# Kernel tuning notes

Hardware: AMD Instinct MI355X
Metric: run time of the kernel (lower is better)

The kernel has to match this reference:

```python
import jax, jax.numpy as jnp
import numpy as np

N0, N1, N2 = 100000, 20000, 4000   # src(block0), dst(block0)=src(block1), dst(block1)
R = 3                               # number of relations
E0, E1 = 160000, 64000              # edges per relation per block
IN_FEATS, HID = 128, 128
TSS, RS = 64, 64
NTOT = 200000                       # global node count for tss/rs embed tables
F_IN = HID + TSS + RS               # IGConv input feature dim = 256


def _lin(key, fi, fo):
    k1, k2 = jax.random.split(key)
    s = float(1.0 / np.sqrt(fi))
    w = jax.random.uniform(k1, (fi, fo), minval=-s, maxval=s, dtype=jnp.float32)
    b = jax.random.uniform(k2, (fo,), minval=-s, maxval=s, dtype=jnp.float32)
    return w, b


def setup_inputs() -> dict:
    ks = jax.random.split(jax.random.key(0), 32)
    inp = {}
    inp["x_user"] = jax.random.normal(ks[0], (N0, IN_FEATS), dtype=jnp.float32)
    inp["tss_embed"] = jax.random.normal(ks[1], (NTOT, TSS), dtype=jnp.float32)
    inp["rs_embed"] = jax.random.normal(ks[2], (NTOT, RS), dtype=jnp.float32)
    inp["src_nid0"] = jax.random.randint(ks[3], (N0,), 0, NTOT)
    inp["src_nid1"] = jax.random.randint(ks[4], (N1,), 0, NTOT)
    inp["e0_src"] = jax.random.randint(ks[5], (R, E0), 0, N0)
    inp["e0_dst"] = jax.random.randint(ks[6], (R, E0), 0, N1)
    inp["e1_src"] = jax.random.randint(ks[7], (R, E1), 0, N1)
    inp["e1_dst"] = jax.random.randint(ks[8], (R, E1), 0, N2)
    inp["embed_w"], inp["embed_b"] = _lin(ks[9], IN_FEATS, HID)
    i = 10
    for l in (1, 2):
        for nm, fi in (("fc1", F_IN), ("fc2", 3 * F_IN), ("fc3", 2 * HID)):
            pw, pb = zip(*[_lin(jax.random.fold_in(ks[i], r), fi, HID) for r in range(R)])
            inp["l%d_%s_w" % (l, nm)] = jnp.stack(pw)  # [R, fi, HID]
            inp["l%d_%s_b" % (l, nm)] = jnp.stack(pb)  # [R, HID]
            i += 1
    inp["attn_w1"], inp["attn_b1"] = _lin(ks[i], HID, HID)
    inp["attn_w2"] = _lin(ks[i + 1], HID, 1)[0]  # Linear(hid,1,bias=False)
    inp["pred_w"], inp["pred_b"] = _lin(ks[i + 2], HID, 1)
    return inp


def _igconv(src_feat, dst_feat, esrc, edst, n_dst, fc1w, fc1b, fc2w, fc2b, fc3w, fc3b):
    # copy_u gather then max/mean/sum segment reductions over destination nodes
    m = src_feat[esrc]                                   # [E, F]
    s = jax.ops.segment_sum(m, edst, num_segments=n_dst)
    deg = jax.ops.segment_sum(jnp.ones(esrc.shape, m.dtype), edst, num_segments=n_dst)
    mean = s / jnp.maximum(deg, 1.0)[:, None]
    mx = jax.ops.segment_max(m, edst, num_segments=n_dst)
    mx = jnp.where(deg[:, None] > 0, mx, jnp.zeros_like(mx))  # DGL zeros for isolated dst
    msg = jnp.concatenate([mx, mean, s], axis=1)         # [n_dst, 3F]
    inp = jnp.concatenate([msg @ fc2w + fc2b, dst_feat @ fc1w + fc1b], axis=1)
    return jax.nn.relu(inp) @ fc3w + fc3b                # [n_dst, HID]


def _attn(z, w1, b1, w2):
    # SemanticAttention: z [N, R, HID]
    w = (jnp.tanh(z @ w1 + b1) @ w2).mean(0)             # [R, 1]
    beta = jax.nn.softmax(w, axis=0)                     # [R, 1]
    return (beta[None] * z).sum(1)                       # [N, HID]


def _forward(x_user, tss_embed, rs_embed, embed_w, embed_b,
             l1_fc1_w, l1_fc1_b, l1_fc2_w, l1_fc2_b, l1_fc3_w, l1_fc3_b,
             l2_fc1_w, l2_fc1_b, l2_fc2_w, l2_fc2_b, l2_fc3_w, l2_fc3_b,
             attn_w1, attn_b1, attn_w2, pred_w, pred_b,
             src_nid0, src_nid1, e0_src, e0_dst, e1_src, e1_dst):
    u0 = x_user @ embed_w + embed_b                      # self.embed
    feat0 = jnp.concatenate([u0, tss_embed[src_nid0], rs_embed[src_nid0]], axis=1)  # [N0,256]
    conv1 = jax.vmap(lambda es, ed, w1, b1, w2, b2, w3, b3:
                     _igconv(feat0, feat0[:N1], es, ed, N1, w1, b1, w2, b2, w3, b3))
    z1 = conv1(e0_src, e0_dst, l1_fc1_w, l1_fc1_b, l1_fc2_w, l1_fc2_b, l1_fc3_w, l1_fc3_b)  # [R,N1,HID]
    h1 = jax.nn.relu(_attn(jnp.transpose(z1, (1, 0, 2)), attn_w1, attn_b1, attn_w2))  # [N1,HID]
    feat1 = jnp.concatenate([h1, tss_embed[src_nid1], rs_embed[src_nid1]], axis=1)    # [N1,256]
    conv2 = jax.vmap(lambda es, ed, w1, b1, w2, b2, w3, b3:
                     _igconv(feat1, feat1[:N2], es, ed, N2, w1, b1, w2, b2, w3, b3))
    z2 = conv2(e1_src, e1_dst, l2_fc1_w, l2_fc1_b, l2_fc2_w, l2_fc2_b, l2_fc3_w, l2_fc3_b)  # [R,N2,HID]
    h2 = _attn(jnp.transpose(z2, (1, 0, 2)), attn_w1, attn_b1, attn_w2)              # [N2,HID]
    return jax.nn.sigmoid(h2 @ pred_w + pred_b)          # [N2,1]


def reference(x_user, tss_embed, rs_embed, src_nid0, src_nid1,
              e0_src, e0_dst, e1_src, e1_dst, embed_w, embed_b,
              l1_fc1_w, l1_fc1_b, l1_fc2_w, l1_fc2_b, l1_fc3_w, l1_fc3_b,
              l2_fc1_w, l2_fc1_b, l2_fc2_w, l2_fc2_b, l2_fc3_w, l2_fc3_b,
              attn_w1, attn_b1, attn_w2, pred_w, pred_b):
    return _forward(x_user, tss_embed, rs_embed, embed_w, embed_b,
                    l1_fc1_w, l1_fc1_b, l1_fc2_w, l1_fc2_b, l1_fc3_w, l1_fc3_b,
                    l2_fc1_w, l2_fc1_b, l2_fc2_w, l2_fc2_b, l2_fc3_w, l2_fc3_b,
                    attn_w1, attn_b1, attn_w2, pred_w, pred_b,
                    src_nid0, src_nid1, e0_src, e0_dst, e1_src, e1_dst)
```

## Files before the change

kernel.cpp:

```cpp
#include <hip/hip_runtime.h>
#include <math.h>


typedef short s16x8 __attribute__((ext_vector_type(8)));
typedef float f32x4 __attribute__((ext_vector_type(4)));

__device__ __forceinline__ ushort f2bf(float f) {
  unsigned u = __float_as_uint(f);
  return (ushort)((u + 0x7FFFu + ((u >> 16) & 1u)) >> 16);
}
__device__ __forceinline__ float bf2f(unsigned hbits) {
  return __uint_as_float(hbits << 16);
}
__device__ __forceinline__ unsigned pack2(float lo, float hi) {
  return (unsigned)f2bf(lo) | ((unsigned)f2bf(hi) << 16);
}

struct PrepAll {
  const float* src[8];
  ushort* dst[8];
  int K[8];
  int total[8];
};

__global__ __launch_bounds__(256) void prep_all(PrepAll P)
{
  int t = blockIdx.z;
  int off = blockIdx.x * 256 + threadIdx.x;
  if (off >= P.total[t]) return;
  int K = P.K[t];
  int k = off % K;
  int n = (off / K) & 127;
  int r = off / (K * 128);
  P.dst[t][off] = f2bf(P.src[t][((size_t)r * K + k) * 128 + n]);
}

struct GemmDesc {
  const void* A; int lda; size_t aStride; int aKind;
  const ushort* Wt; size_t wStride;
  const float* bias; int biasStride;
  void* C; int ldc; size_t cStride; int cKind;
  int M, K, relu;
  const ushort* aggM; const ushort* aggS; const float* invdeg;
  size_t aggStride; int invStride;
  const int* gnid; const float* gtss; const float* grs;
};

template<int AKIND>
__device__ __forceinline__ uint4 loadA(const void* Ab, const ushort* AgM,
                                       const ushort* AgS, int lda, int row,
                                       bool rowOK, int k0, int quad, float idg)
{
  uint4 pk = make_uint4(0u, 0u, 0u, 0u);
  if (rowOK) {
    if constexpr (AKIND == 1) {
      pk = *(const uint4*)((const ushort*)Ab + (size_t)row * lda + k0 + quad * 8);
    } else if constexpr (AKIND == 0) {
      const float* A32 = (const float*)Ab;
      float4 fa = *(const float4*)(A32 + (size_t)row * lda + k0 + quad * 8);
      float4 fb = *(const float4*)(A32 + (size_t)row * lda + k0 + quad * 8 + 4);
      pk.x = pack2(fa.x, fa.y); pk.y = pack2(fa.z, fa.w);
      pk.z = pack2(fb.x, fb.y); pk.w = pack2(fb.z, fb.w);
    } else {
      int seg = k0 >> 8;
      int jj  = (k0 & 255) + quad * 8;
      const ushort* Ag = (seg == 0) ? AgM : AgS;
      pk = *(const uint4*)(Ag + (size_t)row * 256 + jj);
      if (seg == 1) {
        pk.x = pack2(bf2f(pk.x & 0xFFFFu) * idg, bf2f(pk.x >> 16) * idg);
        pk.y = pack2(bf2f(pk.y & 0xFFFFu) * idg, bf2f(pk.y >> 16) * idg);
        pk.z = pack2(bf2f(pk.z & 0xFFFFu) * idg, bf2f(pk.z >> 16) * idg);
        pk.w = pack2(bf2f(pk.w & 0xFFFFu) * idg, bf2f(pk.w >> 16) * idg);
      }
    }
  }
  return pk;
}

template<int K, int AKIND>
__device__ __forceinline__ void gemm_core(const GemmDesc& d, int r, ushort* Bs)
{
  constexpr int NC = K / 64;
  constexpr int NF = K / 32;

  const int tid = threadIdx.x;
  const int wave = tid >> 6, lane = tid & 63;
  const int m16 = lane & 15, quad = lane >> 4;
  const int rowBase = blockIdx.x * 64;
  const int row = rowBase + wave * 16 + m16;
  const bool rowOK = row < d.M;
  const ushort* Wt = d.Wt + (size_t)r * d.wStride;

  const void* Ab = (const char*)d.A +
      (size_t)r * d.aStride * (AKIND == 0 ? sizeof(float) : sizeof(ushort));
  const ushort* AgM = d.aggM + (size_t)r * d.aggStride;
  const ushort* AgS = d.aggS + (size_t)r * d.aggStride;

  float idg = 1.f;
  if (AKIND == 2 && rowOK) idg = d.invdeg[(size_t)r * d.invStride + row];

  f32x4 acc[8];
  #pragma unroll
  for (int j = 0; j < 8; ++j)
    #pragma unroll
    for (int p = 0; p < 4; ++p) acc[j][p] = 0.f;

  uint4 pkAll[(K <= 256) ? NF : 2];
  if constexpr (K <= 256) {
    #pragma unroll
    for (int f = 0; f < NF; ++f)
      pkAll[f] = loadA<AKIND>(Ab, AgM, AgS, d.lda, row, rowOK, f * 32, quad, idg);
  }

  #pragma unroll
  for (int c = 0; c < NC; ++c) {
    if constexpr (K > 256) {
      pkAll[0] = loadA<AKIND>(Ab, AgM, AgS, d.lda, row, rowOK, c * 64,      quad, idg);
      pkAll[1] = loadA<AKIND>(Ab, AgM, AgS, d.lda, row, rowOK, c * 64 + 32, quad, idg);
    }
    if (c) __syncthreads();
    #pragma unroll
    for (int i = 0; i < 4; ++i) {
      int q = tid + 256 * i;
      int col = ((q >> 6) & 7) * 16 + (q & 15);
      int kk  = c * 64 + ((q >> 9) & 1) * 32 + ((q >> 4) & 3) * 8;
      *(uint4*)&Bs[q * 8] = *(const uint4*)(Wt + (size_t)col * K + kk);
    }
    __syncthreads();

    #pragma unroll
    for (int ks = 0; ks < 2; ++ks) {
      uint4 pk = (K <= 256) ? pkAll[c * 2 + ks] : pkAll[ks];
      s16x8 af = *(s16x8*)&pk;
      #pragma unroll
      for (int j = 0; j < 8; ++j) {
        s16x8 bf = *(const s16x8*)&Bs[((ks * 8 + j) * 64 + lane) * 8];
        acc[j] = __builtin_amdgcn_mfma_f32_16x16x32_bf16(af, bf, acc[j], 0, 0, 0);
      }
    }
  }

  const float* bias = d.bias + (size_t)r * d.biasStride;
  float bcol[8];
  #pragma unroll
  for (int j = 0; j < 8; ++j) bcol[j] = bias[j * 16 + m16];

  #pragma unroll
  for (int p = 0; p < 4; ++p) {
    int grow = rowBase + wave * 16 + quad * 4 + p;
    if (grow >= d.M) continue;
    if (d.cKind == 0) {
      float* Crow = (float*)d.C + (size_t)r * d.cStride + (size_t)grow * d.ldc;
      #pragma unroll
      for (int j = 0; j < 8; ++j) {
        float v = acc[j][p] + bcol[j];
        if (d.relu) v = fmaxf(v, 0.f);
        Crow[j * 16 + m16] = v;
      }
    } else {
      ushort* Crow = (ushort*)d.C + (size_t)r * d.cStride + (size_t)grow * d.ldc;
      #pragma unroll
      for (int j = 0; j < 8; ++j) {
        float v = acc[j][p] + bcol[j];
        if (d.relu) v = fmaxf(v, 0.f);
        Crow[j * 16 + m16] = f2bf(v);
      }
    }
  }

  if constexpr (K == 128) {
    if (d.gnid) {
      #pragma unroll
      for (int i = 0; i < 8; ++i) {
        int q = tid + 256 * i;
        int grow = rowBase + (q >> 5);
        int c = q & 31;
        if (grow >= d.M) continue;
        int id = d.gnid[grow];
        float4 v = (c < 16) ? *(const float4*)(d.gtss + (size_t)id * 64 + c * 4)
                            : *(const float4*)(d.grs  + (size_t)id * 64 + (c - 16) * 4);
        uint2 g; g.x = pack2(v.x, v.y); g.y = pack2(v.z, v.w);
        *(uint2*)((ushort*)d.C + (size_t)grow * d.ldc + 128 + c * 4) = g;
      }
    }
  }
}

__global__ __launch_bounds__(256, 4) void gemm_mfma(GemmDesc d0, GemmDesc d1)
{
  __shared__ __align__(16) ushort Bs[1024 * 8];
  const GemmDesc& d = blockIdx.z ? d1 : d0;
  const int r = blockIdx.y;
  if (d.K == 128)      gemm_core<128, 0>(d, r, Bs);
  else if (d.K == 256) gemm_core<256, 1>(d, r, Bs);
  else                 gemm_core<768, 2>(d, r, Bs);
}

__global__ __launch_bounds__(256) void fc3_attn(
    const ushort* __restrict__ inp, size_t aStride,
    const ushort* __restrict__ wt3, size_t wStride,
    const float* __restrict__ b3,
    float* __restrict__ z, size_t zStride, int M,
    const ushort* __restrict__ w1t, const float* __restrict__ b1,
    const float* __restrict__ w2, float* __restrict__ wsum)
{
  __shared__ __align__(16) ushort Zs[64 * 128];
  __shared__ __align__(16) ushort Ws[1024 * 8];

  const int tid = threadIdx.x;
  const int wave = tid >> 6, lane = tid & 63;
  const int m16 = lane & 15, quad = lane >> 4;
  const int r = blockIdx.y;
  const int rowBase = blockIdx.x * 64;
  const int row = rowBase + wave * 16 + m16;
  const bool rowOK = row < M;

  const ushort* A  = inp + (size_t)r * aStride;
  const ushort* Wt = wt3 + (size_t)r * wStride;

  f32x4 acc[8];
  #pragma unroll
  for (int j = 0; j < 8; ++j)
    #pragma unroll
    for (int p = 0; p < 4; ++p) acc[j][p] = 0.f;

  uint4 pkAll[8];
  #pragma unroll
  for (int f = 0; f < 8; ++f) {
    uint4 pk = make_uint4(0u, 0u, 0u, 0u);
    if (rowOK) pk = *(const uint4*)(A + (size_t)row * 256 + f * 32 + quad * 8);
    pkAll[f] = pk;
  }

  #pragma unroll
  for (int c = 0; c < 4; ++c) {
    if (c) __syncthreads();
    #pragma unroll
    for (int i = 0; i < 4; ++i) {
      int q = tid + 256 * i;
      int col = ((q >> 6) & 7) * 16 + (q & 15);
      int kk  = c * 64 + ((q >> 9) & 1) * 32 + ((q >> 4) & 3) * 8;
      *(uint4*)&Ws[q * 8] = *(const uint4*)(Wt + (size_t)col * 256 + kk);
    }
    __syncthreads();
    #pragma unroll
    for (int ks = 0; ks < 2; ++ks) {
      s16x8 af = *(s16x8*)&pkAll[c * 2 + ks];
      #pragma unroll
      for (int j = 0; j < 8; ++j) {
        s16x8 bf = *(const s16x8*)&Ws[((ks * 8 + j) * 64 + lane) * 8];
        acc[j] = __builtin_amdgcn_mfma_f32_16x16x32_bf16(af, bf, acc[j], 0, 0, 0);
      }
    }
  }

  const float* bias = b3 + (size_t)r * 128;
  float bcol[8];
  #pragma unroll
  for (int j = 0; j < 8; ++j) bcol[j] = bias[j * 16 + m16];

  #pragma unroll
  for (int p = 0; p < 4; ++p) {
    int lrow = wave * 16 + quad * 4 + p;
    int grow = rowBase + lrow;
    bool ok = grow < M;
    float* Zr = z + (size_t)r * zStride + (size_t)grow * 128;
    #pragma unroll
    for (int j = 0; j < 8; ++j) {
      float v = ok ? acc[j][p] + bcol[j] : 0.f;
      if (ok) Zr[j * 16 + m16] = v;
      int byte = lrow * 256 + (j * 16 + m16) * 2;
      byte ^= (lrow & 7) << 4;
      *(ushort*)((char*)Zs + byte) = f2bf(v);
    }
  }

  f32x4 acc2[8];
  #pragma unroll
  for (int j = 0; j < 8; ++j)
    #pragma unroll
    for (int p = 0; p < 4; ++p) acc2[j][p] = 0.f;

  const int arow = wave * 16 + m16;
  #pragma unroll
  for (int c = 0; c < 2; ++c) {
    __syncthreads();
    #pragma unroll
    for (int i = 0; i < 4; ++i) {
      int q = tid + 256 * i;
      int col = ((q >> 6) & 7) * 16 + (q & 15);
      int kk  = c * 64 + ((q >> 9) & 1) * 32 + ((q >> 4) & 3) * 8;
      *(uint4*)&Ws[q * 8] = *(const uint4*)(w1t + (size_t)col * 128 + kk);
    }
    __syncthreads();
    #pragma unroll
    for (int ks = 0; ks < 2; ++ks) {
      int kk = c * 64 + ks * 32 + quad * 8;
      int byte = arow * 256 + kk * 2;
      byte ^= (arow & 7) << 4;
      s16x8 af = *(const s16x8*)((const char*)Zs + byte);
      #pragma unroll
      for (int j = 0; j < 8; ++j) {
        s16x8 bf = *(const s16x8*)&Ws[((ks * 8 + j) * 64 + lane) * 8];
        acc2[j] = __builtin_amdgcn_mfma_f32_16x16x32_bf16(af, bf, acc2[j], 0, 0, 0);
      }
    }
  }

  float b1c[8], w2c[8];
  #pragma unroll
  for (int j = 0; j < 8; ++j) { b1c[j] = b1[j * 16 + m16]; w2c[j] = w2[j * 16 + m16]; }

  float local = 0.f;
  #pragma unroll
  for (int p = 0; p < 4; ++p) {
    int grow = rowBase + wave * 16 + quad * 4 + p;
    if (grow >= M) continue;
    #pragma unroll
    for (int j = 0; j < 8; ++j)
      local += tanhf(acc2[j][p] + b1c[j]) * w2c[j];
  }
  #pragma unroll
  for (int o = 32; o > 0; o >>= 1) local += __shfl_down(local, o);
  __shared__ float red[4];
  if (lane == 0) red[wave] = local;
  __syncthreads();
  if (tid == 0) atomicAdd(&wsum[r], red[0] + red[1] + red[2] + red[3]);
}

__global__ void count_deg(const int* __restrict__ edst, int E, int N, int* __restrict__ deg)
{
  int e = blockIdx.x * blockDim.x + threadIdx.x;
  int r = blockIdx.y;
  if (e < E) atomicAdd(&deg[r * N + edst[(size_t)r * E + e]], 1);
}

__global__ __launch_bounds__(1024) void scan_kernel(
    const int* __restrict__ deg, int* __restrict__ rowptr,
    int* __restrict__ cursor, int N)
{
  const int r = blockIdx.y;
  const int* dg = deg + (size_t)r * N;
  int* rp  = rowptr + (size_t)r * (N + 1);
  int* cur = cursor + (size_t)r * N;

  __shared__ int wtot[16];
  __shared__ int chunk_total_s;
  const int tid = threadIdx.x, lane = tid & 63, wid = tid >> 6;
  int running = 0;
  for (int base = 0; base < N; base += 4096) {
    int i0 = base + tid * 4;
    int d0 = 0, d1 = 0, d2 = 0, d3 = 0;
    if (i0 < N) {
      if (i0 + 3 < N) { int4 t = *(const int4*)(dg + i0); d0 = t.x; d1 = t.y; d2 = t.z; d3 = t.w; }
      else { d0 = dg[i0]; if (i0+1 < N) d1 = dg[i0+1]; if (i0+2 < N) d2 = dg[i0+2]; }
    }
    int tsum = d0 + d1 + d2 + d3;
    int incl = tsum;
    #pragma unroll
    for (int o = 1; o < 64; o <<= 1) {
      int t = __shfl_up(incl, o);
      if (lane >= o) incl += t;
    }
    if (lane == 63) wtot[wid] = incl;
    __syncthreads();
    if (wid == 0 && lane < 16) {
      int t = wtot[lane];
      int inc = t;
      #pragma unroll
      for (int o = 1; o < 16; o <<= 1) {
        int u = __shfl_up(inc, o);
        if (lane >= o) inc += u;
      }
      wtot[lane] = inc - t;
      if (lane == 15) chunk_total_s = inc;
    }
    __syncthreads();
    int excl = running + wtot[wid] + (incl - tsum);
    if (i0 < N) {
      int e1 = excl + d0, e2 = e1 + d1, e3 = e2 + d2;
      if (i0 + 3 < N) {
        *(int4*)(rp + i0) = make_int4(excl, e1, e2, e3);
        *(int4*)(cur + i0) = make_int4(0, 0, 0, 0);
      } else {
        rp[i0] = excl; cur[i0] = 0;
        if (i0+1 < N) { rp[i0+1] = e1; cur[i0+1] = 0; }
        if (i0+2 < N) { rp[i0+2] = e2; cur[i0+2] = 0; }
      }
    }
    running += chunk_total_s;
    __syncthreads();
  }
  if (tid == 0) rp[N] = running;
}

__global__ void fill_csr(const int* __restrict__ esrc, const int* __restrict__ edst,
                         int E, int N, const int* __restrict__ rowptr,
                         int* __restrict__ cursor, int* __restrict__ csr)
{
  int e = blockIdx.x * blockDim.x + threadIdx.x;
  int r = blockIdx.y;
  if (e >= E) return;
  int dn = edst[(size_t)r * E + e];
  int pos = atomicAdd(&cursor[r * N + dn], 1);
  csr[(size_t)r * E + rowptr[(size_t)r * (N + 1) + dn] + pos] = esrc[(size_t)r * E + e];
}

__global__ __launch_bounds__(256) void agg_kernel(
    const ushort* __restrict__ feat, const int* __restrict__ csr,
    const int* __restrict__ rowptr, int N, int c0, int cr, int CH, int E,
    ushort* __restrict__ aggS, ushort* __restrict__ aggM, float* __restrict__ invdeg)
{
  const int wid = threadIdx.x >> 6, lane = threadIdx.x & 63;
  const int node = blockIdx.x * 4 + wid;
  if (node >= cr) return;
  const size_t rp = (size_t)blockIdx.y * (N + 1) + c0 + node;
  const int o = blockIdx.y * CH + node;
  const int start = rowptr[rp], end = rowptr[rp + 1];
  const int* ecsr = csr + (size_t)blockIdx.y * E;
  const int j = lane * 4;
  float s0 = 0.f, s1 = 0.f, s2 = 0.f, s3 = 0.f;
  float m0 = -INFINITY, m1 = -INFINITY, m2 = -INFINITY, m3 = -INFINITY;
  int e = start;
  for (; e + 4 <= end; e += 4) {
    int sa = ecsr[e], sb = ecsr[e+1], sc = ecsr[e+2], sd = ecsr[e+3];
    uint2 va = *(const uint2*)(feat + (size_t)sa * 256 + j);
    uint2 vb = *(const uint2*)(feat + (size_t)sb * 256 + j);
    uint2 vc = *(const uint2*)(feat + (size_t)sc * 256 + j);
    uint2 vd = *(const uint2*)(feat + (size_t)sd * 256 + j);
    float a0, a1, a2, a3;
    a0 = bf2f(va.x & 0xFFFFu); a1 = bf2f(va.x >> 16); a2 = bf2f(va.y & 0xFFFFu); a3 = bf2f(va.y >> 16);
    s0 += a0; s1 += a1; s2 += a2; s3 += a3;
    m0 = fmaxf(m0, a0); m1 = fmaxf(m1, a1); m2 = fmaxf(m2, a2); m3 = fmaxf(m3, a3);
    a0 = bf2f(vb.x & 0xFFFFu); a1 = bf2f(vb.x >> 16); a2 = bf2f(vb.y & 0xFFFFu); a3 = bf2f(vb.y >> 16);
    s0 += a0; s1 += a1; s2 += a2; s3 += a3;
    m0 = fmaxf(m0, a0); m1 = fmaxf(m1, a1); m2 = fmaxf(m2, a2); m3 = fmaxf(m3, a3);
    a0 = bf2f(vc.x & 0xFFFFu); a1 = bf2f(vc.x >> 16); a2 = bf2f(vc.y & 0xFFFFu); a3 = bf2f(vc.y >> 16);
    s0 += a0; s1 += a1; s2 += a2; s3 += a3;
    m0 = fmaxf(m0, a0); m1 = fmaxf(m1, a1); m2 = fmaxf(m2, a2); m3 = fmaxf(m3, a3);
    a0 = bf2f(vd.x & 0xFFFFu); a1 = bf2f(vd.x >> 16); a2 = bf2f(vd.y & 0xFFFFu); a3 = bf2f(vd.y >> 16);
    s0 += a0; s1 += a1; s2 += a2; s3 += a3;
    m0 = fmaxf(m0, a0); m1 = fmaxf(m1, a1); m2 = fmaxf(m2, a2); m3 = fmaxf(m3, a3);
  }
  for (; e < end; ++e) {
    int src = ecsr[e];
    uint2 v = *(const uint2*)(feat + (size_t)src * 256 + j);
    float a0 = bf2f(v.x & 0xFFFFu), a1 = bf2f(v.x >> 16);
    float a2 = bf2f(v.y & 0xFFFFu), a3 = bf2f(v.y >> 16);
    s0 += a0; s1 += a1; s2 += a2; s3 += a3;
    m0 = fmaxf(m0, a0); m1 = fmaxf(m1, a1); m2 = fmaxf(m2, a2); m3 = fmaxf(m3, a3);
  }
  if (end == start) { m0 = m1 = m2 = m3 = 0.f; }
  uint2 ps; ps.x = pack2(s0, s1); ps.y = pack2(s2, s3);
  *(uint2*)(aggS + (size_t)o * 256 + j) = ps;
  uint2 pm; pm.x = pack2(m0, m1); pm.y = pack2(m2, m3);
  *(uint2*)(aggM + (size_t)o * 256 + j) = pm;
  if (lane == 0) invdeg[o] = 1.f / fmaxf((float)(end - start), 1.f);
}

__global__ void beta_kernel(const float* __restrict__ wsum, float invN, float* __restrict__ beta) {
  float w0 = wsum[0] * invN, w1 = wsum[1] * invN, w2 = wsum[2] * invN;
  float m  = fmaxf(w0, fmaxf(w1, w2));
  float e0 = expf(w0 - m), e1 = expf(w1 - m), e2 = expf(w2 - m);
  float s  = e0 + e1 + e2;
  beta[0] = e0 / s; beta[1] = e1 / s; beta[2] = e2 / s;
}

__global__ __launch_bounds__(256) void combine1_kernel(
    const float* __restrict__ z1, const float* __restrict__ beta,
    const float* __restrict__ tss, const float* __restrict__ rs,
    const int* __restrict__ nid, int N, ushort* __restrict__ feat1)
{
  int n = blockIdx.x, t = threadIdx.x;
  size_t NH = (size_t)N * 128;
  if (t < 128) {
    float v = beta[0] * z1[(size_t)n*128 + t] + beta[1] * z1[NH + (size_t)n*128 + t]
            + beta[2] * z1[2*NH + (size_t)n*128 + t];
    feat1[(size_t)n*256 + t] = f2bf(fmaxf(v, 0.f));
  } else {
    int j = t - 128;
    int id = nid[n];
    float v = (j < 64) ? tss[(size_t)id*64 + j] : rs[(size_t)id*64 + j - 64];
    feat1[(size_t)n*256 + t] = f2bf(v);
  }
}

__global__ __launch_bounds__(128) void combine2_pred(
    const float* __restrict__ z2, const float* __restrict__ beta, int N,
    const float* __restrict__ pw, const float* __restrict__ pb, float* __restrict__ out)
{
  int n = blockIdx.x, t = threadIdx.x;
  size_t NH = (size_t)N * 128;
  float h = beta[0] * z2[(size_t)n*128 + t] + beta[1] * z2[NH + (size_t)n*128 + t]
          + beta[2] * z2[2*NH + (size_t)n*128 + t];
  float p = h * pw[t];
  #pragma unroll
  for (int o = 32; o > 0; o >>= 1) p += __shfl_down(p, o);
  __shared__ float red[2];
  if ((t & 63) == 0) red[t >> 6] = p;
  __syncthreads();
  if (t == 0) {
    float v = red[0] + red[1] + pb[0];
    out[n] = 1.f / (1.f + expf(-v));
  }
}

extern "C" void kernel_launch(void* const* d_in, const int* in_sizes, int n_in,
                              void* d_out, int out_size, void* d_ws, size_t ws_size,
                              hipStream_t stream)
{
  const float* x_user  = (const float*)d_in[0];
  const float* tss     = (const float*)d_in[1];
  const float* rs      = (const float*)d_in[2];
  const int* src_nid0  = (const int*)d_in[3];
  const int* src_nid1  = (const int*)d_in[4];
  const int* e0_src    = (const int*)d_in[5];
  const int* e0_dst    = (const int*)d_in[6];
  const int* e1_src    = (const int*)d_in[7];
  const int* e1_dst    = (const int*)d_in[8];
  const float* embed_w = (const float*)d_in[9];
  const float* embed_b = (const float*)d_in[10];
  const float* l1w[3]  = {(const float*)d_in[11], (const float*)d_in[13], (const float*)d_in[15]};
  const float* l1b[3]  = {(const float*)d_in[12], (const float*)d_in[14], (const float*)d_in[16]};
  const float* l2w[3]  = {(const float*)d_in[17], (const float*)d_in[19], (const float*)d_in[21]};
  const float* l2b[3]  = {(const float*)d_in[18], (const float*)d_in[20], (const float*)d_in[22]};
  const float* attn_w1 = (const float*)d_in[23];
  const float* attn_b1 = (const float*)d_in[24];
  const float* attn_w2 = (const float*)d_in[25];
  const float* pred_w  = (const float*)d_in[26];
  const float* pred_b  = (const float*)d_in[27];
  float* out = (float*)d_out;

  const int N0 = in_sizes[0] / 128;
  const int N1 = in_sizes[4];
  const int N2 = out_size;
  const int E0 = in_sizes[5] / 3;
  const int E1 = in_sizes[7] / 3;

  char* wp = (char*)d_ws;
  auto walloc = [&](size_t bytes) {
    char* p = wp; wp += (bytes + 255) & ~(size_t)255; return p;
  };
  ushort* feat0  = (ushort*)walloc((size_t)N0 * 256 * 2);
  ushort* inp    = (ushort*)walloc((size_t)3 * N1 * 256 * 2);
  float*  z      = (float*)walloc((size_t)3 * N1 * 128 * 4);
  ushort* wt_emb = (ushort*)walloc((size_t)128 * 128 * 2);
  ushort* wt_attn = (ushort*)walloc((size_t)128 * 128 * 2);
  ushort* wt_fc1[2], *wt_fc2[2], *wt_fc3[2];
  for (int l = 0; l < 2; ++l) {
    wt_fc1[l] = (ushort*)walloc((size_t)3 * 256 * 128 * 2);
    wt_fc2[l] = (ushort*)walloc((size_t)3 * 768 * 128 * 2);
    wt_fc3[l] = (ushort*)walloc((size_t)3 * 256 * 128 * 2);
  }
  int*   degcnt = (int*)walloc((size_t)3 * N1 * 4);
  int*   rowptr = (int*)walloc((size_t)3 * (N1 + 1) * 4);
  int*   csr    = (int*)walloc((size_t)3 * E0 * 4);
  float* small  = (float*)walloc(256);
  float* wsum = small;
  float* beta = small + 4;
  ushort* feat1 = feat0;

  size_t used = (size_t)(wp - (char*)d_ws);
  size_t avail = (ws_size > used + 65536) ? (ws_size - used - 65536) : 0;
  const size_t per_row = (size_t)3 * (2 * 256 * 2 + 4 + 64);
  int CH = (int)(avail / per_row);
  if (CH > N1) CH = N1;
  if (CH < 1024) CH = 1024;
  ushort* aggS   = (ushort*)walloc((size_t)3 * CH * 256 * 2);
  ushort* aggM   = (ushort*)walloc((size_t)3 * CH * 256 * 2);
  float*  invdeg = (float*)walloc((size_t)3 * CH * 4);
  (void)n_in;

  {
    PrepAll P;
    P.src[0] = embed_w;  P.dst[0] = wt_emb;    P.K[0] = 128; P.total[0] = 128 * 128;
    P.src[1] = attn_w1;  P.dst[1] = wt_attn;   P.K[1] = 128; P.total[1] = 128 * 128;
    P.src[2] = l1w[0];   P.dst[2] = wt_fc1[0]; P.K[2] = 256; P.total[2] = 3 * 256 * 128;
    P.src[3] = l1w[1];   P.dst[3] = wt_fc2[0]; P.K[3] = 768; P.total[3] = 3 * 768 * 128;
    P.src[4] = l1w[2];   P.dst[4] = wt_fc3[0]; P.K[4] = 256; P.total[4] = 3 * 256 * 128;
    P.src[5] = l2w[0];   P.dst[5] = wt_fc1[1]; P.K[5] = 256; P.total[5] = 3 * 256 * 128;
    P.src[6] = l2w[1];   P.dst[6] = wt_fc2[1]; P.K[6] = 768; P.total[6] = 3 * 768 * 128;
    P.src[7] = l2w[2];   P.dst[7] = wt_fc3[1]; P.K[7] = 256; P.total[7] = 3 * 256 * 128;
    prep_all<<<dim3((3 * 768 * 128 + 255) / 256, 1, 8), 256, 0, stream>>>(P);
  }

  GemmDesc dz = {};
  dz.K = 256;

  {
    GemmDesc d{};
    d.A = x_user; d.lda = 128; d.aStride = 0; d.aKind = 0;
    d.Wt = wt_emb; d.wStride = 0; d.bias = embed_b; d.biasStride = 0;
    d.C = feat0; d.ldc = 256; d.cStride = 0; d.cKind = 1;
    d.M = N0; d.K = 128; d.relu = 0;
    d.aggM = aggM; d.aggS = aggS; d.invdeg = invdeg; d.aggStride = 0; d.invStride = 0;
    d.gnid = src_nid0; d.gtss = tss; d.grs = rs;
    gemm_mfma<<<dim3((N0 + 63) / 64, 1, 1), 256, 0, stream>>>(d, dz);
  }

  for (int layer = 0; layer < 2; ++layer) {
    const ushort* featS = layer ? feat1 : feat0;
    int Nd = layer ? N2 : N1;
    int E  = layer ? E1 : E0;
    const int* es = layer ? e1_src : e0_src;
    const int* ed = layer ? e1_dst : e0_dst;
    const float* const* lb = layer ? l2b : l1b;

    hipMemsetAsync(degcnt, 0, (size_t)3 * Nd * 4, stream);
    count_deg<<<dim3((E + 255) / 256, 3), 256, 0, stream>>>(ed, E, Nd, degcnt);
    scan_kernel<<<dim3(1, 3), 1024, 0, stream>>>(degcnt, rowptr, degcnt, Nd);
    fill_csr<<<dim3((E + 255) / 256, 3), 256, 0, stream>>>(es, ed, E, Nd, rowptr, degcnt, csr);

    for (int c0 = 0; c0 < Nd; c0 += CH) {
      int cr = (Nd - c0 < CH) ? (Nd - c0) : CH;
      agg_kernel<<<dim3((cr + 3) / 4, 3), 256, 0, stream>>>(
          featS, csr, rowptr, Nd, c0, cr, CH, E, aggS, aggM, invdeg);
      GemmDesc d2{};
      d2.A = nullptr; d2.lda = 0; d2.aStride = 0; d2.aKind = 2;
      d2.Wt = wt_fc2[layer]; d2.wStride = (size_t)768 * 128; d2.bias = lb[1]; d2.biasStride = 128;
      d2.C = inp + (size_t)c0 * 256; d2.ldc = 256; d2.cStride = (size_t)Nd * 256; d2.cKind = 1;
      d2.M = cr; d2.K = 768; d2.relu = 1;
      d2.aggM = aggM; d2.aggS = aggS; d2.invdeg = invdeg;
      d2.aggStride = (size_t)CH * 256; d2.invStride = CH;
      GemmDesc d1{};
      d1.A = featS + (size_t)c0 * 256; d1.lda = 256; d1.aStride = 0; d1.aKind = 1;
      d1.Wt = wt_fc1[layer]; d1.wStride = (size_t)256 * 128; d1.bias = lb[0]; d1.biasStride = 128;
      d1.C = inp + 128 + (size_t)c0 * 256; d1.ldc = 256; d1.cStride = (size_t)Nd * 256; d1.cKind = 1;
      d1.M = cr; d1.K = 256; d1.relu = 1;
      d1.aggM = aggM; d1.aggS = aggS; d1.invdeg = invdeg; d1.aggStride = 0; d1.invStride = 0;
      gemm_mfma<<<dim3((cr + 63) / 64, 3, 2), 256, 0, stream>>>(d2, d1);
    }

    hipMemsetAsync(wsum, 0, 3 * sizeof(float), stream);
    fc3_attn<<<dim3((Nd + 63) / 64, 3), 256, 0, stream>>>(
        inp, (size_t)Nd * 256, wt_fc3[layer], (size_t)256 * 128, lb[2],
        z, (size_t)Nd * 128, Nd, wt_attn, attn_b1, attn_w2, wsum);
    beta_kernel<<<1, 1, 0, stream>>>(wsum, 1.0f / (float)Nd, beta);

    if (layer == 0) {
      combine1_kernel<<<N1, 256, 0, stream>>>(z, beta, tss, rs, src_nid1, N1, feat1);
    } else {
      combine2_pred<<<N2, 128, 0, stream>>>(z, beta, N2, pred_w, pred_b, out);
    }
  }
}
```

Baseline: 522.5 us.

## Use persistent embed GEMM kernel and vectorize combine kernels

Replaces the generic MFMA GEMM path for the input embedding with a dedicated persistent kernel. Each block loads the full 128x128 bf16 weight into LDS once, then its waves loop over 16-row tiles, converting fp32 activations to bf16 in registers and fusing the tss/rs gather. The combine1 and combine2_pred kernels are rewritten so each 32-lane group handles one node with float4 loads and a 32-wide shuffle reduction, instead of one block per node. The aim is to cut the repeated weight staging and per-node launch granularity; the cost is more register pressure and a separate code path.

```diff
diff --git a/kernel.cpp b/kernel.cpp
--- a/kernel.cpp
+++ b/kernel.cpp
@@ -33,6 +33,92 @@
   int n = (off / K) & 127;
   int r = off / (K * 128);
   P.dst[t][off] = f2bf(P.src[t][((size_t)r * K + k) * 128 + n]);
+}
+
+__global__ __launch_bounds__(256) void embed_gemm(
+    const float* __restrict__ A, const ushort* __restrict__ Wt,
+    const float* __restrict__ bias, ushort* __restrict__ C, int M, int nt,
+    const int* __restrict__ gnid, const float* __restrict__ gtss,
+    const float* __restrict__ grs)
+{
+  __shared__ __align__(16) ushort Bs[2048 * 8];
+  const int tid = threadIdx.x;
+  const int lane = tid & 63;
+  const int m16 = lane & 15, quad = lane >> 4;
+
+  #pragma unroll
+  for (int i = 0; i < 8; ++i) {
+    int q = tid + 256 * i;
+    int col = ((q >> 6) & 7) * 16 + (q & 15);
+    int kk  = (q >> 9) * 32 + ((q >> 4) & 3) * 8;
+    *(uint4*)&Bs[q * 8] = *(const uint4*)(Wt + (size_t)col * 128 + kk);
+  }
+  __syncthreads();
+
+  float bcol[8];
+  #pragma unroll
+  for (int j = 0; j < 8; ++j) bcol[j] = bias[j * 16 + m16];
+
+  const int gwave = blockIdx.x * 4 + (tid >> 6);
+  const int nwaves = gridDim.x * 4;
+
+  for (int t = gwave; t < nt; t += nwaves) {
+    const int row0 = t * 16;
+    const int row = row0 + m16;
+    const bool rowOK = row < M;
+
+    uint4 pk[4];
+    #pragma unroll
+    for (int f = 0; f < 4; ++f) {
+      uint4 v = make_uint4(0u, 0u, 0u, 0u);
+      if (rowOK) {
+        float4 fa = *(const float4*)(A + (size_t)row * 128 + f * 32 + quad * 8);
+        float4 fb = *(const float4*)(A + (size_t)row * 128 + f * 32 + quad * 8 + 4);
+        v.x = pack2(fa.x, fa.y); v.y = pack2(fa.z, fa.w);
+        v.z = pack2(fb.x, fb.y); v.w = pack2(fb.z, fb.w);
+      }
+      pk[f] = v;
+    }
+
+    f32x4 acc[8];
+    #pragma unroll
+    for (int j = 0; j < 8; ++j)
+      #pragma unroll
+      for (int p = 0; p < 4; ++p) acc[j][p] = 0.f;
+
+    #pragma unroll
+    for (int f = 0; f < 4; ++f) {
+      s16x8 af = *(s16x8*)&pk[f];
+      #pragma unroll
+      for (int j = 0; j < 8; ++j) {
+        s16x8 bf = *(const s16x8*)&Bs[((f * 8 + j) * 64 + lane) * 8];
+        acc[j] = __builtin_amdgcn_mfma_f32_16x16x32_bf16(af, bf, acc[j], 0, 0, 0);
+      }
+    }
+
+    #pragma unroll
+    for (int p = 0; p < 4; ++p) {
+      int grow = row0 + quad * 4 + p;
+      if (grow >= M) continue;
+      ushort* Crow = C + (size_t)grow * 256;
+      #pragma unroll
+      for (int j = 0; j < 8; ++j)
+        Crow[j * 16 + m16] = f2bf(acc[j][p] + bcol[j]);
+    }
+
+    #pragma unroll
+    for (int i = 0; i < 8; ++i) {
+      int q = lane + 64 * i;
+      int grow = row0 + (q >> 5);
+      int c = q & 31;
+      if (grow >= M) continue;
+      int id = gnid[grow];
+      float4 v = (c < 16) ? *(const float4*)(gtss + (size_t)id * 64 + c * 4)
+                          : *(const float4*)(grs  + (size_t)id * 64 + (c - 16) * 4);
+      uint2 g; g.x = pack2(v.x, v.y); g.y = pack2(v.z, v.w);
+      *(uint2*)(C + (size_t)grow * 256 + 128 + c * 4) = g;
+    }
+  }
 }
 
 struct GemmDesc {
@@ -167,23 +253,6 @@
       }
     }
   }
-
-  if constexpr (K == 128) {
-    if (d.gnid) {
-      #pragma unroll
-      for (int i = 0; i < 8; ++i) {
-        int q = tid + 256 * i;
-        int grow = rowBase + (q >> 5);
-        int c = q & 31;
-        if (grow >= d.M) continue;
-        int id = d.gnid[grow];
-        float4 v = (c < 16) ? *(const float4*)(d.gtss + (size_t)id * 64 + c * 4)
-                            : *(const float4*)(d.grs  + (size_t)id * 64 + (c - 16) * 4);
-        uint2 g; g.x = pack2(v.x, v.y); g.y = pack2(v.z, v.w);
-        *(uint2*)((ushort*)d.C + (size_t)grow * d.ldc + 128 + c * 4) = g;
-      }
-    }
-  }
 }
 
 __global__ __launch_bounds__(256, 4) void gemm_mfma(GemmDesc d0, GemmDesc d1)
@@ -191,8 +260,7 @@
   __shared__ __align__(16) ushort Bs[1024 * 8];
   const GemmDesc& d = blockIdx.z ? d1 : d0;
   const int r = blockIdx.y;
-  if (d.K == 128)      gemm_core<128, 0>(d, r, Bs);
-  else if (d.K == 256) gemm_core<256, 1>(d, r, Bs);
+  if (d.K == 256)      gemm_core<256, 1>(d, r, Bs);
   else                 gemm_core<768, 2>(d, r, Bs);
 }
 
@@ -471,38 +539,52 @@
     const float* __restrict__ tss, const float* __restrict__ rs,
     const int* __restrict__ nid, int N, ushort* __restrict__ feat1)
 {
-  int n = blockIdx.x, t = threadIdx.x;
+  int n = blockIdx.x * 8 + (threadIdx.x >> 5);
+  int c = threadIdx.x & 31;
+  if (n >= N) return;
   size_t NH = (size_t)N * 128;
-  if (t < 128) {
-    float v = beta[0] * z1[(size_t)n*128 + t] + beta[1] * z1[NH + (size_t)n*128 + t]
-            + beta[2] * z1[2*NH + (size_t)n*128 + t];
-    feat1[(size_t)n*256 + t] = f2bf(fmaxf(v, 0.f));
-  } else {
-    int j = t - 128;
-    int id = nid[n];
-    float v = (j < 64) ? tss[(size_t)id*64 + j] : rs[(size_t)id*64 + j - 64];
-    feat1[(size_t)n*256 + t] = f2bf(v);
-  }
-}
-
-__global__ __launch_bounds__(128) void combine2_pred(
+  float b0 = beta[0], b1 = beta[1], b2 = beta[2];
+  const float* zp = z1 + (size_t)n * 128 + c * 4;
+  float4 v0 = *(const float4*)zp;
+  float4 v1 = *(const float4*)(zp + NH);
+  float4 v2 = *(const float4*)(zp + 2 * NH);
+  float wx = fmaxf(b0 * v0.x + b1 * v1.x + b2 * v2.x, 0.f);
+  float wy = fmaxf(b0 * v0.y + b1 * v1.y + b2 * v2.y, 0.f);
+  float wz = fmaxf(b0 * v0.z + b1 * v1.z + b2 * v2.z, 0.f);
+  float ww = fmaxf(b0 * v0.w + b1 * v1.w + b2 * v2.w, 0.f);
+  uint2 g; g.x = pack2(wx, wy); g.y = pack2(wz, ww);
+  *(uint2*)(feat1 + (size_t)n * 256 + c * 4) = g;
+  int id = nid[n];
+  float4 t = (c < 16) ? *(const float4*)(tss + (size_t)id * 64 + c * 4)
+                      : *(const float4*)(rs  + (size_t)id * 64 + (c - 16) * 4);
+  uint2 g2; g2.x = pack2(t.x, t.y); g2.y = pack2(t.z, t.w);
+  *(uint2*)(feat1 + (size_t)n * 256 + 128 + c * 4) = g2;
+}
+
+__global__ __launch_bounds__(256) void combine2_pred(
     const float* __restrict__ z2, const float* __restrict__ beta, int N,
     const float* __restrict__ pw, const float* __restrict__ pb, float* __restrict__ out)
 {
-  int n = blockIdx.x, t = threadIdx.x;
-  size_t NH = (size_t)N * 128;
-  float h = beta[0] * z2[(size_t)n*128 + t] + beta[1] * z2[NH + (size_t)n*128 + t]
-          + beta[2] * z2[2*NH + (size_t)n*128 + t];
-  float p = h * pw[t];
-  #pragma unroll
-  for (int o = 32; o > 0; o >>= 1) p += __shfl_down(p, o);
-  __shared__ float red[2];
-  if ((t & 63) == 0) red[t >> 6] = p;
-  __syncthreads();
-  if (t == 0) {
-    float v = red[0] + red[1] + pb[0];
-    out[n] = 1.f / (1.f + expf(-v));
-  }
+  int n = blockIdx.x * 8 + (threadIdx.x >> 5);
+  int c = threadIdx.x & 31;
+  bool ok = n < N;
+  float p = 0.f;
+  if (ok) {
+    size_t NH = (size_t)N * 128;
+    const float* zp = z2 + (size_t)n * 128 + c * 4;
+    float4 v0 = *(const float4*)zp;
+    float4 v1 = *(const float4*)(zp + NH);
+    float4 v2 = *(const float4*)(zp + 2 * NH);
+    float4 w = *(const float4*)(pw + c * 4);
+    float b0 = beta[0], b1 = beta[1], b2 = beta[2];
+    p  = (b0 * v0.x + b1 * v1.x + b2 * v2.x) * w.x;
+    p += (b0 * v0.y + b1 * v1.y + b2 * v2.y) * w.y;
+    p += (b0 * v0.z + b1 * v1.z + b2 * v2.z) * w.z;
+    p += (b0 * v0.w + b1 * v1.w + b2 * v2.w) * w.w;
+  }
+  #pragma unroll
+  for (int o = 16; o > 0; o >>= 1) p += __shfl_down(p, o, 32);
+  if (ok && c == 0) out[n] = 1.f / (1.f + expf(-(p + pb[0])));
 }
 
 extern "C" void kernel_launch(void* const* d_in, const int* in_sizes, int n_in,
@@ -584,19 +666,16 @@
     prep_all<<<dim3((3 * 768 * 128 + 255) / 256, 1, 8), 256, 0, stream>>>(P);
   }
 
+  {
+    int nt = (N0 + 15) / 16;
+    int blocks = 1280;
+    if (blocks * 4 > nt) blocks = (nt + 3) / 4;
+    embed_gemm<<<blocks, 256, 0, stream>>>(
+        x_user, wt_emb, embed_b, feat0, N0, nt, src_nid0, tss, rs);
+  }
+
   GemmDesc dz = {};
   dz.K = 256;
-
-  {
-    GemmDesc d{};
-    d.A = x_user; d.lda = 128; d.aStride = 0; d.aKind = 0;
-    d.Wt = wt_emb; d.wStride = 0; d.bias = embed_b; d.biasStride = 0;
-    d.C = feat0; d.ldc = 256; d.cStride = 0; d.cKind = 1;
-    d.M = N0; d.K = 128; d.relu = 0;
-    d.aggM = aggM; d.aggS = aggS; d.invdeg = invdeg; d.aggStride = 0; d.invStride = 0;
-    d.gnid = src_nid0; d.gtss = tss; d.grs = rs;
-    gemm_mfma<<<dim3((N0 + 63) / 64, 1, 1), 256, 0, stream>>>(d, dz);
-  }
 
   for (int layer = 0; layer < 2; ++layer) {
     const ushort* featS = layer ? feat1 : feat0;
@@ -638,9 +717,9 @@
     beta_kernel<<<1, 1, 0, stream>>>(wsum, 1.0f / (float)Nd, beta);
 
     if (layer == 0) {
-      combine1_kernel<<<N1, 256, 0, stream>>>(z, beta, tss, rs, src_nid1, N1, feat1);
+      combine1_kernel<<<(N1 + 7) / 8, 256, 0, stream>>>(z, beta, tss, rs, src_nid1, N1, feat1);
     } else {
-      combine2_pred<<<N2, 128, 0, stream>>>(z, beta, N2, pred_w, pred_b, out);
-    }
-  }
-}
+      combine2_pred<<<(N2 + 7) / 8, 256, 0, stream>>>(z, beta, N2, pred_w, pred_b, out);
+    }
+  }
+}
```

Result: no change. 527.7 us (+1.0%).

## Batch CSR builds for both layers, fold beta into combine kernels

Applied to the files above, without the earlier changes.

Builds the CSR for both layers in one set of count/scan/fill launches over 6 relation slices, and clears all counters and wsum with a single memset. The separate beta kernel is removed: each combine kernel now computes the softmax weights from wsum itself. The combine kernels are rewritten to handle 8 nodes per block with float4 loads. The aim is fewer launches and memsets plus better-coalesced combine loads, at the cost of a larger workspace holding both CSRs.

```diff
diff --git a/kernel.cpp b/kernel.cpp
--- a/kernel.cpp
+++ b/kernel.cpp
@@ -328,21 +328,31 @@
   if (tid == 0) atomicAdd(&wsum[r], red[0] + red[1] + red[2] + red[3]);
 }
 
-__global__ void count_deg(const int* __restrict__ edst, int E, int N, int* __restrict__ deg)
-{
-  int e = blockIdx.x * blockDim.x + threadIdx.x;
-  int r = blockIdx.y;
-  if (e < E) atomicAdd(&deg[r * N + edst[(size_t)r * E + e]], 1);
-}
-
-__global__ __launch_bounds__(1024) void scan_kernel(
-    const int* __restrict__ deg, int* __restrict__ rowptr,
-    int* __restrict__ cursor, int N)
-{
-  const int r = blockIdx.y;
-  const int* dg = deg + (size_t)r * N;
-  int* rp  = rowptr + (size_t)r * (N + 1);
-  int* cur = cursor + (size_t)r * N;
+struct Csr6 {
+  const int* edst0; const int* edst1;
+  const int* esrc0; const int* esrc1;
+  int E0, E1, N1, N2;
+  int* deg;
+  int* rowptr;
+  int* csr;
+};
+
+__global__ void count_deg6(Csr6 c)
+{
+  int y = blockIdx.y, l = y / 3, r = y - l * 3;
+  int E = l ? c.E1 : c.E0, N = l ? c.N2 : c.N1;
+  const int* ed = l ? c.edst1 : c.edst0;
+  int* deg = c.deg + (l ? 3 * c.N1 : 0) + r * N;
+  int e = blockIdx.x * 256 + threadIdx.x;
+  if (e < E) atomicAdd(&deg[ed[(size_t)r * E + e]], 1);
+}
+
+__global__ __launch_bounds__(1024) void scan_kernel6(Csr6 c)
+{
+  int y = blockIdx.y, l = y / 3, r = y - l * 3;
+  int N = l ? c.N2 : c.N1;
+  int* dgm = c.deg + (l ? 3 * c.N1 : 0) + r * N;
+  int* rp  = c.rowptr + (l ? 3 * (c.N1 + 1) : 0) + r * (N + 1);
 
   __shared__ int wtot[16];
   __shared__ int chunk_total_s;
@@ -352,8 +362,8 @@
     int i0 = base + tid * 4;
     int d0 = 0, d1 = 0, d2 = 0, d3 = 0;
     if (i0 < N) {
-      if (i0 + 3 < N) { int4 t = *(const int4*)(dg + i0); d0 = t.x; d1 = t.y; d2 = t.z; d3 = t.w; }
-      else { d0 = dg[i0]; if (i0+1 < N) d1 = dg[i0+1]; if (i0+2 < N) d2 = dg[i0+2]; }
+      if (i0 + 3 < N) { int4 t = *(const int4*)(dgm + i0); d0 = t.x; d1 = t.y; d2 = t.z; d3 = t.w; }
+      else { d0 = dgm[i0]; if (i0+1 < N) d1 = dgm[i0+1]; if (i0+2 < N) d2 = dgm[i0+2]; }
     }
     int tsum = d0 + d1 + d2 + d3;
     int incl = tsum;
@@ -381,11 +391,11 @@
       int e1 = excl + d0, e2 = e1 + d1, e3 = e2 + d2;
       if (i0 + 3 < N) {
         *(int4*)(rp + i0) = make_int4(excl, e1, e2, e3);
-        *(int4*)(cur + i0) = make_int4(0, 0, 0, 0);
+        *(int4*)(dgm + i0) = make_int4(0, 0, 0, 0);
       } else {
-        rp[i0] = excl; cur[i0] = 0;
-        if (i0+1 < N) { rp[i0+1] = e1; cur[i0+1] = 0; }
-        if (i0+2 < N) { rp[i0+2] = e2; cur[i0+2] = 0; }
+        rp[i0] = excl; dgm[i0] = 0;
+        if (i0+1 < N) { rp[i0+1] = e1; dgm[i0+1] = 0; }
+        if (i0+2 < N) { rp[i0+2] = e2; dgm[i0+2] = 0; }
       }
     }
     running += chunk_total_s;
@@ -394,16 +404,20 @@
   if (tid == 0) rp[N] = running;
 }
 
-__global__ void fill_csr(const int* __restrict__ esrc, const int* __restrict__ edst,
-                         int E, int N, const int* __restrict__ rowptr,
-                         int* __restrict__ cursor, int* __restrict__ csr)
-{
-  int e = blockIdx.x * blockDim.x + threadIdx.x;
-  int r = blockIdx.y;
+__global__ void fill_csr6(Csr6 c)
+{
+  int y = blockIdx.y, l = y / 3, r = y - l * 3;
+  int E = l ? c.E1 : c.E0, N = l ? c.N2 : c.N1;
+  const int* ed = l ? c.edst1 : c.edst0;
+  const int* es = l ? c.esrc1 : c.esrc0;
+  int* cur = c.deg + (l ? 3 * c.N1 : 0) + r * N;
+  const int* rp = c.rowptr + (l ? 3 * (c.N1 + 1) : 0) + r * (N + 1);
+  int* csr = c.csr + (l ? 3 * c.E0 : 0) + (size_t)r * E;
+  int e = blockIdx.x * 256 + threadIdx.x;
   if (e >= E) return;
-  int dn = edst[(size_t)r * E + e];
-  int pos = atomicAdd(&cursor[r * N + dn], 1);
-  csr[(size_t)r * E + rowptr[(size_t)r * (N + 1) + dn] + pos] = esrc[(size_t)r * E + e];
+  int dn = ed[(size_t)r * E + e];
+  int pos = atomicAdd(&cur[dn], 1);
+  csr[rp[dn] + pos] = es[(size_t)r * E + e];
 }
 
 __global__ __launch_bounds__(256) void agg_kernel(
@@ -458,51 +472,70 @@
   if (lane == 0) invdeg[o] = 1.f / fmaxf((float)(end - start), 1.f);
 }
 
-__global__ void beta_kernel(const float* __restrict__ wsum, float invN, float* __restrict__ beta) {
+__device__ __forceinline__ void beta_from_wsum(const float* wsum, float invN,
+                                               float& b0, float& b1, float& b2)
+{
   float w0 = wsum[0] * invN, w1 = wsum[1] * invN, w2 = wsum[2] * invN;
   float m  = fmaxf(w0, fmaxf(w1, w2));
   float e0 = expf(w0 - m), e1 = expf(w1 - m), e2 = expf(w2 - m);
-  float s  = e0 + e1 + e2;
-  beta[0] = e0 / s; beta[1] = e1 / s; beta[2] = e2 / s;
+  float s  = 1.f / (e0 + e1 + e2);
+  b0 = e0 * s; b1 = e1 * s; b2 = e2 * s;
 }
 
 __global__ __launch_bounds__(256) void combine1_kernel(
-    const float* __restrict__ z1, const float* __restrict__ beta,
+    const float* __restrict__ z1, const float* __restrict__ wsum, float invN,
     const float* __restrict__ tss, const float* __restrict__ rs,
     const int* __restrict__ nid, int N, ushort* __restrict__ feat1)
 {
-  int n = blockIdx.x, t = threadIdx.x;
+  int n = blockIdx.x * 8 + (threadIdx.x >> 5);
+  int c = threadIdx.x & 31;
+  if (n >= N) return;
+  float b0, b1, b2;
+  beta_from_wsum(wsum, invN, b0, b1, b2);
   size_t NH = (size_t)N * 128;
-  if (t < 128) {
-    float v = beta[0] * z1[(size_t)n*128 + t] + beta[1] * z1[NH + (size_t)n*128 + t]
-            + beta[2] * z1[2*NH + (size_t)n*128 + t];
-    feat1[(size_t)n*256 + t] = f2bf(fmaxf(v, 0.f));
-  } else {
-    int j = t - 128;
-    int id = nid[n];
-    float v = (j < 64) ? tss[(size_t)id*64 + j] : rs[(size_t)id*64 + j - 64];
-    feat1[(size_t)n*256 + t] = f2bf(v);
-  }
-}
-
-__global__ __launch_bounds__(128) void combine2_pred(
-    const float* __restrict__ z2, const float* __restrict__ beta, int N,
-    const float* __restrict__ pw, const float* __restrict__ pb, float* __restrict__ out)
-{
-  int n = blockIdx.x, t = threadIdx.x;
-  size_t NH = (size_t)N * 128;
-  float h = beta[0] * z2[(size_t)n*128 + t] + beta[1] * z2[NH + (size_t)n*128 + t]
-          + beta[2] * z2[2*NH + (size_t)n*128 + t];
-  float p = h * pw[t];
-  #pragma unroll
-  for (int o = 32; o > 0; o >>= 1) p += __shfl_down(p, o);
-  __shared__ float red[2];
-  if ((t & 63) == 0) red[t >> 6] = p;
-  __syncthreads();
-  if (t == 0) {
-    float v = red[0] + red[1] + pb[0];
-    out[n] = 1.f / (1.f + expf(-v));
-  }
+  const float* zp = z1 + (size_t)n * 128 + c * 4;
+  float4 v0 = *(const float4*)zp;
+  float4 v1 = *(const float4*)(zp + NH);
+  float4 v2 = *(const float4*)(zp + 2 * NH);
+  float wx = fmaxf(b0 * v0.x + b1 * v1.x + b2 * v2.x, 0.f);
+  float wy = fmaxf(b0 * v0.y + b1 * v1.y + b2 * v2.y, 0.f);
+  float wz = fmaxf(b0 * v0.z + b1 * v1.z + b2 * v2.z, 0.f);
+  float ww = fmaxf(b0 * v0.w + b1 * v1.w + b2 * v2.w, 0.f);
+  uint2 g; g.x = pack2(wx, wy); g.y = pack2(wz, ww);
+  *(uint2*)(feat1 + (size_t)n * 256 + c * 4) = g;
+  int id = nid[n];
+  float4 t = (c < 16) ? *(const float4*)(tss + (size_t)id * 64 + c * 4)
+                      : *(const float4*)(rs  + (size_t)id * 64 + (c - 16) * 4);
+  uint2 g2; g2.x = pack2(t.x, t.y); g2.y = pack2(t.z, t.w);
+  *(uint2*)(feat1 + (size_t)n * 256 + 128 + c * 4) = g2;
+}
+
+__global__ __launch_bounds__(256) void combine2_pred(
+    const float* __restrict__ z2, const float* __restrict__ wsum, float invN,
+    int N, const float* __restrict__ pw, const float* __restrict__ pb,
+    float* __restrict__ out)
+{
+  int n = blockIdx.x * 8 + (threadIdx.x >> 5);
+  int c = threadIdx.x & 31;
+  bool ok = n < N;
+  float p = 0.f;
+  if (ok) {
+    float b0, b1, b2;
+    beta_from_wsum(wsum, invN, b0, b1, b2);
+    size_t NH = (size_t)N * 128;
+    const float* zp = z2 + (size_t)n * 128 + c * 4;
+    float4 v0 = *(const float4*)zp;
+    float4 v1 = *(const float4*)(zp + NH);
+    float4 v2 = *(const float4*)(zp + 2 * NH);
+    float4 w = *(const float4*)(pw + c * 4);
+    p  = (b0 * v0.x + b1 * v1.x + b2 * v2.x) * w.x;
+    p += (b0 * v0.y + b1 * v1.y + b2 * v2.y) * w.y;
+    p += (b0 * v0.z + b1 * v1.z + b2 * v2.z) * w.z;
+    p += (b0 * v0.w + b1 * v1.w + b2 * v2.w) * w.w;
+  }
+  #pragma unroll
+  for (int o = 16; o > 0; o >>= 1) p += __shfl_down(p, o, 32);
+  if (ok && c == 0) out[n] = 1.f / (1.f + expf(-(p + pb[0])));
 }
 
 extern "C" void kernel_launch(void* const* d_in, const int* in_sizes, int n_in,
@@ -552,12 +585,12 @@
     wt_fc2[l] = (ushort*)walloc((size_t)3 * 768 * 128 * 2);
     wt_fc3[l] = (ushort*)walloc((size_t)3 * 256 * 128 * 2);
   }
-  int*   degcnt = (int*)walloc((size_t)3 * N1 * 4);
-  int*   rowptr = (int*)walloc((size_t)3 * (N1 + 1) * 4);
-  int*   csr    = (int*)walloc((size_t)3 * E0 * 4);
+  size_t degBytes = ((size_t)3 * (N1 + N2) * 4 + 255) & ~(size_t)255;
+  int*   degcnt = (int*)walloc(degBytes);
   float* small  = (float*)walloc(256);
+  int*   rowptr = (int*)walloc((size_t)(3 * (N1 + 1) + 3 * (N2 + 1)) * 4);
+  int*   csr    = (int*)walloc((size_t)3 * (E0 + E1) * 4);
   float* wsum = small;
-  float* beta = small + 4;
   ushort* feat1 = feat0;
 
   size_t used = (size_t)(wp - (char*)d_ws);
@@ -570,6 +603,8 @@
   ushort* aggM   = (ushort*)walloc((size_t)3 * CH * 256 * 2);
   float*  invdeg = (float*)walloc((size_t)3 * CH * 4);
   (void)n_in;
+
+  hipMemsetAsync(degcnt, 0, degBytes + 256, stream);
 
   {
     PrepAll P;
@@ -598,23 +633,31 @@
     gemm_mfma<<<dim3((N0 + 63) / 64, 1, 1), 256, 0, stream>>>(d, dz);
   }
 
+  Csr6 c6;
+  c6.edst0 = e0_dst; c6.edst1 = e1_dst;
+  c6.esrc0 = e0_src; c6.esrc1 = e1_src;
+  c6.E0 = E0; c6.E1 = E1; c6.N1 = N1; c6.N2 = N2;
+  c6.deg = degcnt; c6.rowptr = rowptr; c6.csr = csr;
+  {
+    int Emax = E0 > E1 ? E0 : E1;
+    count_deg6<<<dim3((Emax + 255) / 256, 6), 256, 0, stream>>>(c6);
+    scan_kernel6<<<dim3(1, 6), 1024, 0, stream>>>(c6);
+    fill_csr6<<<dim3((Emax + 255) / 256, 6), 256, 0, stream>>>(c6);
+  }
+
   for (int layer = 0; layer < 2; ++layer) {
     const ushort* featS = layer ? feat1 : feat0;
     int Nd = layer ? N2 : N1;
     int E  = layer ? E1 : E0;
-    const int* es = layer ? e1_src : e0_src;
-    const int* ed = layer ? e1_dst : e0_dst;
     const float* const* lb = layer ? l2b : l1b;
-
-    hipMemsetAsync(degcnt, 0, (size_t)3 * Nd * 4, stream);
-    count_deg<<<dim3((E + 255) / 256, 3), 256, 0, stream>>>(ed, E, Nd, degcnt);
-    scan_kernel<<<dim3(1, 3), 1024, 0, stream>>>(degcnt, rowptr, degcnt, Nd);
-    fill_csr<<<dim3((E + 255) / 256, 3), 256, 0, stream>>>(es, ed, E, Nd, rowptr, degcnt, csr);
+    const int* rp_l  = rowptr + (layer ? 3 * (N1 + 1) : 0);
+    const int* csr_l = csr + (layer ? 3 * E0 : 0);
+    float* wsum_l = wsum + 3 * layer;
 
     for (int c0 = 0; c0 < Nd; c0 += CH) {
       int cr = (Nd - c0 < CH) ? (Nd - c0) : CH;
       agg_kernel<<<dim3((cr + 3) / 4, 3), 256, 0, stream>>>(
-          featS, csr, rowptr, Nd, c0, cr, CH, E, aggS, aggM, invdeg);
+          featS, csr_l, rp_l, Nd, c0, cr, CH, E, aggS, aggM, invdeg);
       GemmDesc d2{};
       d2.A = nullptr; d2.lda = 0; d2.aStride = 0; d2.aKind = 2;
       d2.Wt = wt_fc2[layer]; d2.wStride = (size_t)768 * 128; d2.bias = lb[1]; d2.biasStride = 128;
@@ -631,16 +674,16 @@
       gemm_mfma<<<dim3((cr + 63) / 64, 3, 2), 256, 0, stream>>>(d2, d1);
     }
 
-    hipMemsetAsync(wsum, 0, 3 * sizeof(float), stream);
     fc3_attn<<<dim3((Nd + 63) / 64, 3), 256, 0, stream>>>(
         inp, (size_t)Nd * 256, wt_fc3[layer], (size_t)256 * 128, lb[2],
-        z, (size_t)Nd * 128, Nd, wt_attn, attn_b1, attn_w2, wsum);
-    beta_kernel<<<1, 1, 0, stream>>>(wsum, 1.0f / (float)Nd, beta);
+        z, (size_t)Nd * 128, Nd, wt_attn, attn_b1, attn_w2, wsum_l);
 
     if (layer == 0) {
-      combine1_kernel<<<N1, 256, 0, stream>>>(z, beta, tss, rs, src_nid1, N1, feat1);
+      combine1_kernel<<<(N1 + 7) / 8, 256, 0, stream>>>(
+          z, wsum_l, 1.0f / (float)N1, tss, rs, src_nid1, N1, feat1);
     } else {
-      combine2_pred<<<N2, 128, 0, stream>>>(z, beta, N2, pred_w, pred_b, out);
-    }
-  }
-}
+      combine2_pred<<<(N2 + 7) / 8, 256, 0, stream>>>(
+          z, wsum_l, 1.0f / (float)N2, N2, pred_w, pred_b, out);
+    }
+  }
+}
```

New measurement: 497.8 us. 1.05x faster.
